# Optimization experiments

Hardware: AMD Instinct MI355X
Metric: run time of the kernel (lower is better)

The kernel has to match this reference:

```python
import jax, jax.numpy as jnp
import numpy as np

D_MODEL = 2048
NUM_Q_HEADS = 16
NUM_KV_HEADS = 4
HEAD_DIM = D_MODEL // NUM_Q_HEADS  # 128
NUM_GROUPS = NUM_Q_HEADS // NUM_KV_HEADS  # 4
ROPE_BASE = 10000.0


def _rope_cos_sin(seq_len, head_dim):
    inv_freq = 1.0 / (ROPE_BASE ** (jnp.arange(0, head_dim, 2, dtype=jnp.float32) / head_dim))
    t = jnp.arange(seq_len, dtype=jnp.float32)
    freqs = jnp.outer(t, inv_freq)            # [S, head_dim/2]
    emb = jnp.concatenate([freqs, freqs], -1)  # [S, head_dim]
    return jnp.cos(emb)[None, :, None, :], jnp.sin(emb)[None, :, None, :]


def _rotate_half(x):
    half = x.shape[-1] // 2
    return jnp.concatenate([-x[..., half:], x[..., :half]], axis=-1)


def setup_inputs() -> dict:
    key = jax.random.key(0)
    k0, k1, k2, k3, k4 = jax.random.split(key, 5)
    B, S = 2, 2048
    kv_dim = HEAD_DIM * NUM_KV_HEADS
    scale = D_MODEL ** -0.5
    return {
        "x": jax.random.normal(k0, (B, S, D_MODEL), jnp.float32),
        "attention_mask": jnp.ones((B, S), jnp.int32),
        "Wq": jax.random.normal(k1, (D_MODEL, D_MODEL), jnp.float32) * scale,
        "Wk": jax.random.normal(k2, (D_MODEL, kv_dim), jnp.float32) * scale,
        "Wv": jax.random.normal(k3, (D_MODEL, kv_dim), jnp.float32) * scale,
        "Wo": jax.random.normal(k4, (D_MODEL, D_MODEL), jnp.float32) * scale,
    }


def reference(x, attention_mask, Wq, Wk, Wv, Wo):
    B, S, _ = x.shape
    q = (x @ Wq).reshape(B, S, NUM_Q_HEADS, HEAD_DIM)
    k = (x @ Wk).reshape(B, S, NUM_KV_HEADS, HEAD_DIM)
    v = (x @ Wv).reshape(B, S, NUM_KV_HEADS, HEAD_DIM)

    cos, sin = _rope_cos_sin(S, HEAD_DIM)  # [1,S,1,hd]
    q = q * cos + _rotate_half(q) * sin
    k = k * cos + _rotate_half(k) * sin

    # [B, H, S, hd]; replicate KV heads across groups (repeat_interleave)
    q = q.transpose(0, 2, 1, 3)
    k = jnp.repeat(k.transpose(0, 2, 1, 3), NUM_GROUPS, axis=1)
    v = jnp.repeat(v.transpose(0, 2, 1, 3), NUM_GROUPS, axis=1)

    scale = HEAD_DIM ** -0.5
    scores = jnp.einsum("bhqd,bhkd->bhqk", q, k) * scale
    mask = attention_mask[:, None, None, :]  # [B,1,1,S] over keys
    scores = jnp.where(mask == 0, jnp.float32(-jnp.inf), scores)
    probs = jax.nn.softmax(scores, axis=-1)
    out = jnp.einsum("bhqk,bhkd->bhqd", probs, v)
    out = out.transpose(0, 2, 1, 3).reshape(B, S, D_MODEL)
    return out @ Wo
```

## Files before the change

kernel.cpp:

```cpp
#include <hip/hip_runtime.h>
#include <hip/hip_bf16.h>

typedef __attribute__((ext_vector_type(4))) float f32x4;
typedef __attribute__((ext_vector_type(8))) short s16x8;
typedef __attribute__((ext_vector_type(4))) short s16x4;

__device__ __forceinline__ float fexp2(float x) {
    float y; asm("v_exp_f32 %0, %1" : "=v"(y) : "v"(x)); return y;
}

__global__ void rope_tables(float* __restrict__ cosT, float* __restrict__ sinT) {
    const int s = blockIdx.x, j = threadIdx.x;
    const double inv = pow(10000.0, -(double)j / 64.0);
    const double f = (double)s * inv;
    cosT[s * 64 + j] = (float)cos(f);
    sinT[s * 64 + j] = (float)sin(f);
}

__global__ void mask_bias(const int* __restrict__ mask, float* __restrict__ mb, int n) {
    const int i = blockIdx.x * 256 + threadIdx.x;
    if (i < n) mb[i] = (mask[i] == 0) ? -1e30f : 0.f;
}

__global__ __launch_bounds__(256)
void cast_f32_bf16(const float* __restrict__ src, __hip_bfloat16* __restrict__ dst, int n4) {
    const int i = blockIdx.x * 256 + threadIdx.x;
    if (i < n4) {
        f32x4 v = *reinterpret_cast<const f32x4*>(src + (size_t)i * 4);
        union { s16x4 v4; __hip_bfloat16 h[4]; } u;
#pragma unroll
        for (int j = 0; j < 4; ++j) u.h[j] = __float2bfloat16(v[j]);
        *reinterpret_cast<s16x4*>(dst + (size_t)i * 4) = u.v4;
    }
}

__global__ __launch_bounds__(256)
void transpose_cast(const float* __restrict__ src, __hip_bfloat16* __restrict__ dst,
                    int R, int C) {
    __shared__ __align__(16) float t[32][33];
    const int tx = threadIdx.x, ty = threadIdx.y;
    const int r0 = blockIdx.y * 32, c0 = blockIdx.x * 32;
#pragma unroll
    for (int i = 0; i < 32; i += 8)
        t[ty + i][tx] = src[(size_t)(r0 + ty + i) * C + c0 + tx];
    __syncthreads();
#pragma unroll
    for (int i = 0; i < 32; i += 8)
        dst[(size_t)(c0 + ty + i) * R + r0 + tx] = __float2bfloat16(t[tx][ty + i]);
}

__global__ __launch_bounds__(256)
void vt_transpose(const float* __restrict__ qkv, __hip_bfloat16* __restrict__ Vt) {
    __shared__ __align__(16) float t[32][33];
    const int tx = threadIdx.x, ty = threadIdx.y;
    const int s0 = blockIdx.x * 32, d0 = blockIdx.y * 32;
    const int bh = blockIdx.z, b = bh >> 2, hh = bh & 3;
#pragma unroll
    for (int i = 0; i < 32; i += 8)
        t[ty + i][tx] = qkv[(size_t)(b * 2048 + s0 + ty + i) * 3072 + 2560 + hh * 128 + d0 + tx];
    __syncthreads();
#pragma unroll
    for (int i = 0; i < 32; i += 8)
        Vt[((size_t)(bh * 128) + d0 + ty + i) * 2048 + s0 + tx] = __float2bfloat16(t[tx][ty + i]);
}

template<int NI>
__global__ __launch_bounds__(512, 1)
void gemm256_bt_f32(const __hip_bfloat16* __restrict__ A,
                    const __hip_bfloat16* __restrict__ Bt,
                    float* __restrict__ C, int M, int N, int K) {
    constexpr int NB = NI / 2;
    __shared__ __align__(16) __hip_bfloat16 sm[4][2][8192];
    const int tid = threadIdx.x;
    const int l = tid & 63, w = tid >> 6;
    const int lo = l & 15, hi = l >> 4;
    const int wm = w >> 2, wn = w & 3;
    const int row0 = blockIdx.y * 256;
    const int col0 = blockIdx.x * (NI * 64);
    const int nk = K >> 5;

    f32x4 acc[8][NI];
#pragma unroll
    for (int mi = 0; mi < 8; ++mi)
#pragma unroll
        for (int ni = 0; ni < NI; ++ni) acc[mi][ni] = f32x4{0.f, 0.f, 0.f, 0.f};

    auto stage = [&](int kt) {
        const int s = kt & 3, k0 = kt << 5;
#pragma unroll
        for (int i = 0; i < 2; ++i) {
            const int c = i * 512 + tid;
            const int r = c >> 2, sw = ((c & 3) ^ (r & 3)) * 8;
            __builtin_amdgcn_global_load_lds(
                (const __attribute__((address_space(1))) void*)(A + (size_t)(row0 + r) * K + k0 + sw),
                (__attribute__((address_space(3))) void*)(&sm[s][0][c * 8]), 16, 0, 0);
        }
#pragma unroll
        for (int i = 0; i < NB; ++i) {
            const int c = i * 512 + tid;
            const int r = c >> 2, sw = ((c & 3) ^ (r & 3)) * 8;
            __builtin_amdgcn_global_load_lds(
                (const __attribute__((address_space(1))) void*)(Bt + (size_t)(col0 + r) * K + k0 + sw),
                (__attribute__((address_space(3))) void*)(&sm[s][1][c * 8]), 16, 0, 0);
        }
    };

    stage(0); stage(1); stage(2);
    for (int kt = 0; kt < nk; ++kt) {
        const int s = kt & 3;
        if (kt < nk - 2) {
            if constexpr (NI == 4) asm volatile("s_waitcnt vmcnt(8)" ::: "memory");
            else                   asm volatile("s_waitcnt vmcnt(6)" ::: "memory");
        } else if (kt == nk - 2) {
            if constexpr (NI == 4) asm volatile("s_waitcnt vmcnt(4)" ::: "memory");
            else                   asm volatile("s_waitcnt vmcnt(3)" ::: "memory");
        } else {
            asm volatile("s_waitcnt vmcnt(0)" ::: "memory");
        }
        asm volatile("s_waitcnt lgkmcnt(0)" ::: "memory");
        asm volatile("s_barrier" ::: "memory");
        if (kt + 3 < nk) stage(kt + 3);

        s16x8 af[8], bf[NI];
#pragma unroll
        for (int mi = 0; mi < 8; ++mi)
            af[mi] = *reinterpret_cast<const s16x8*>(
                &sm[s][0][(wm * 128 + mi * 16 + lo) * 32 + ((hi ^ (lo & 3)) * 8)]);
#pragma unroll
        for (int ni = 0; ni < NI; ++ni)
            bf[ni] = *reinterpret_cast<const s16x8*>(
                &sm[s][1][(wn * NI * 16 + ni * 16 + lo) * 32 + ((hi ^ (lo & 3)) * 8)]);
        __builtin_amdgcn_s_setprio(1);
#pragma unroll
        for (int mi = 0; mi < 8; ++mi)
#pragma unroll
            for (int ni = 0; ni < NI; ++ni)
                acc[mi][ni] = __builtin_amdgcn_mfma_f32_16x16x32_bf16(af[mi], bf[ni], acc[mi][ni], 0, 0, 0);
        __builtin_amdgcn_s_setprio(0);
    }
    const int rbase = row0 + wm * 128 + hi * 4;
    const int cbase = col0 + wn * NI * 16 + lo;
#pragma unroll
    for (int mi = 0; mi < 8; ++mi)
#pragma unroll
        for (int ni = 0; ni < NI; ++ni)
#pragma unroll
            for (int r = 0; r < 4; ++r)
                C[(size_t)(rbase + mi * 16 + r) * N + cbase + ni * 16] = acc[mi][ni][r];
}

__global__ __launch_bounds__(256)
void rope_scatter(const float* __restrict__ qkv,
                  const float* __restrict__ cosT, const float* __restrict__ sinT,
                  __hip_bfloat16* __restrict__ Qr, __hip_bfloat16* __restrict__ Kr) {
    const int m = blockIdx.y;
    const int col4 = blockIdx.x * 256 + threadIdx.x;
    if (col4 >= 640) return;
    const int col = col4 * 4;
    const int b = m >> 11, s = m & 2047;
    const int d = col & 127;
    const int j = d & 63;
    const f32x4 v = *reinterpret_cast<const f32x4*>(qkv + (size_t)m * 3072 + col);
    const f32x4 p = *reinterpret_cast<const f32x4*>(qkv + (size_t)m * 3072 + (col ^ 64));
    const f32x4 c4 = *reinterpret_cast<const f32x4*>(cosT + s * 64 + j);
    const f32x4 s4 = *reinterpret_cast<const f32x4*>(sinT + s * 64 + j);
    const float sgn = (d < 64) ? -1.f : 1.f;
    union { s16x4 v4; __hip_bfloat16 h[4]; } u;
#pragma unroll
    for (int i = 0; i < 4; ++i)
        u.h[i] = __float2bfloat16(v[i] * c4[i] + sgn * p[i] * s4[i]);
    if (col < 2048) {
        const int hh = col >> 7;
        *reinterpret_cast<s16x4*>(&Qr[((size_t)(b * 16 + hh) * 2048 + s) * 128 + d]) = u.v4;
    } else {
        const int hh = (col - 2048) >> 7;
        *reinterpret_cast<s16x4*>(&Kr[((size_t)(b * 4 + hh) * 2048 + s) * 128 + d]) = u.v4;
    }
}

__global__ __launch_bounds__(512, 4)
void attn_kernel(const __hip_bfloat16* __restrict__ Qr,
                 const __hip_bfloat16* __restrict__ Kr,
                 const __hip_bfloat16* __restrict__ Vt,
                 const float* __restrict__ maskb,
                 __hip_bfloat16* __restrict__ Oo) {
    const int S = 2048;
    const int qt = blockIdx.x;
    const int bh = blockIdx.y;
    const int b = bh >> 4, h = bh & 15, kvh = h >> 2;
    const int tid = threadIdx.x;
    const int l = tid & 63, w = tid >> 6;
    const int lo = l & 15, hi = l >> 4;
    __shared__ __align__(16) __hip_bfloat16 Ks[2][64 * 128];
    __shared__ __align__(16) __hip_bfloat16 Vs[2][128 * 64];
    __shared__ __align__(16) __hip_bfloat16 Ps[8][16 * 64];

    const __hip_bfloat16* Qb = Qr + (size_t)(b * 16 + h) * S * 128;
    const __hip_bfloat16* Kb = Kr + (size_t)(b * 4 + kvh) * S * 128;
    const __hip_bfloat16* Vb = Vt + (size_t)(b * 4 + kvh) * 128 * S;
    const float* mrow = maskb + b * S;

    const int qrow = qt * 128 + w * 16 + lo;
    s16x8 qf[4];
#pragma unroll
    for (int kc = 0; kc < 4; ++kc)
        qf[kc] = *reinterpret_cast<const s16x8*>(Qb + (size_t)qrow * 128 + kc * 32 + hi * 8);

    float m_run = -1e30f, l_run = 0.f;
    f32x4 o[8];
#pragma unroll
    for (int n = 0; n < 8; ++n) o[n] = f32x4{0.f, 0.f, 0.f, 0.f};
    const float scale2 = 0.12751682f;

    const int krow = tid >> 4, kc8 = tid & 15;
    const int koff = (kc8 ^ (krow & 7)) * 8;
    const int vrow = tid >> 3, vc8 = tid & 7;
    const int voff = (vc8 ^ (vrow & 7)) * 8;

    s16x8 kreg[2], vreg[2];
    auto load_tile = [&](int kv0) {
#pragma unroll
        for (int i = 0; i < 2; ++i)
            kreg[i] = *reinterpret_cast<const s16x8*>(
                Kb + (size_t)(kv0 + i * 32 + krow) * 128 + kc8 * 8);
#pragma unroll
        for (int i = 0; i < 2; ++i)
            vreg[i] = *reinterpret_cast<const s16x8*>(
                Vb + (size_t)(i * 64 + vrow) * S + kv0 + vc8 * 8);
    };

    auto body = [&](int kt, __hip_bfloat16* Kc, __hip_bfloat16* Vc) {
        const int kv0 = kt * 64;
        f32x4 bi[4];
#pragma unroll
        for (int ksub = 0; ksub < 4; ++ksub)
            bi[ksub] = *reinterpret_cast<const f32x4*>(mrow + kv0 + ksub * 16 + hi * 4);
#pragma unroll
        for (int i = 0; i < 2; ++i)
            *reinterpret_cast<s16x8*>(Kc + (i * 32 + krow) * 128 + koff) = kreg[i];
#pragma unroll
        for (int i = 0; i < 2; ++i)
            *reinterpret_cast<s16x8*>(Vc + (i * 64 + vrow) * 64 + voff) = vreg[i];
        if (kt < 31) load_tile(kv0 + 64);
        __syncthreads();

        f32x4 sc[4] = {};
        __builtin_amdgcn_s_setprio(1);
#pragma unroll
        for (int ksub = 0; ksub < 4; ++ksub) {
            const int kr = ksub * 16 + lo;
            const int ksw = kr & 7;
#pragma unroll
            for (int kc = 0; kc < 4; ++kc) {
                s16x8 kf = *reinterpret_cast<const s16x8*>(
                    Kc + kr * 128 + (((kc * 4 + hi) ^ ksw) * 8));
                sc[ksub] = __builtin_amdgcn_mfma_f32_16x16x32_bf16(kf, qf[kc], sc[ksub], 0, 0, 0);
            }
        }
        __builtin_amdgcn_s_setprio(0);
#pragma unroll
        for (int ksub = 0; ksub < 4; ++ksub)
#pragma unroll
            for (int r = 0; r < 4; ++r)
                sc[ksub][r] = fmaf(sc[ksub][r], scale2, bi[ksub][r]);
        float a0 = fmaxf(fmaxf(sc[0][0], sc[0][1]), fmaxf(sc[0][2], sc[0][3]));
        float a1 = fmaxf(fmaxf(sc[1][0], sc[1][1]), fmaxf(sc[1][2], sc[1][3]));
        float a2 = fmaxf(fmaxf(sc[2][0], sc[2][1]), fmaxf(sc[2][2], sc[2][3]));
        float a3 = fmaxf(fmaxf(sc[3][0], sc[3][1]), fmaxf(sc[3][2], sc[3][3]));
        float mx = fmaxf(fmaxf(a0, a1), fmaxf(a2, a3));
        mx = fmaxf(mx, __shfl_xor(mx, 16));
        mx = fmaxf(mx, __shfl_xor(mx, 32));
        if (__ballot(mx > m_run + 11.5417f) != 0ull) {
            const float mnew = fmaxf(m_run, mx);
            const float alpha = fexp2(m_run - mnew);
            m_run = mnew;
            l_run *= alpha;
            float ar[4];
#pragma unroll
            for (int r = 0; r < 4; ++r) ar[r] = __shfl(alpha, hi * 4 + r);
#pragma unroll
            for (int n = 0; n < 8; ++n)
#pragma unroll
                for (int r = 0; r < 4; ++r) o[n][r] *= ar[r];
        }
        float s0 = 0.f, s1 = 0.f, s2 = 0.f, s3 = 0.f;
#pragma unroll
        for (int r = 0; r < 4; ++r) {
            sc[0][r] = fexp2(sc[0][r] - m_run); s0 += sc[0][r];
            sc[1][r] = fexp2(sc[1][r] - m_run); s1 += sc[1][r];
            sc[2][r] = fexp2(sc[2][r] - m_run); s2 += sc[2][r];
            sc[3][r] = fexp2(sc[3][r] - m_run); s3 += sc[3][r];
        }
        float ssum = (s0 + s1) + (s2 + s3);
        ssum += __shfl_xor(ssum, 16);
        ssum += __shfl_xor(ssum, 32);
        l_run += ssum;
        __hip_bfloat16* pb = &Ps[w][0];
#pragma unroll
        for (int ksub = 0; ksub < 4; ++ksub) {
            unsigned int d0, d1;
            asm("v_cvt_pk_bf16_f32 %0, %1, %2" : "=v"(d0) : "v"(sc[ksub][0]), "v"(sc[ksub][1]));
            asm("v_cvt_pk_bf16_f32 %0, %1, %2" : "=v"(d1) : "v"(sc[ksub][2]), "v"(sc[ksub][3]));
            const int byteoff = lo * 128 + (((ksub * 2 + (hi >> 1)) ^ (lo & 7)) * 16) + (hi & 1) * 8;
            uint2 dd; dd.x = d0; dd.y = d1;
            *reinterpret_cast<uint2*>(reinterpret_cast<char*>(pb) + byteoff) = dd;
        }
        __builtin_amdgcn_s_setprio(1);
#pragma unroll
        for (int kg = 0; kg < 2; ++kg) {
            s16x8 pa = *reinterpret_cast<const s16x8*>(
                pb + lo * 64 + (((kg * 4 + hi) ^ (lo & 7)) * 8));
#pragma unroll
            for (int n = 0; n < 8; ++n) {
                const int vr = n * 16 + lo;
                s16x8 vb = *reinterpret_cast<const s16x8*>(
                    Vc + vr * 64 + (((kg * 4 + hi) ^ (vr & 7)) * 8));
                o[n] = __builtin_amdgcn_mfma_f32_16x16x32_bf16(pa, vb, o[n], 0, 0, 0);
            }
        }
        __builtin_amdgcn_s_setprio(0);
    };

    load_tile(0);
    for (int kt2 = 0; kt2 < 16; ++kt2) {
        body(2 * kt2,     &Ks[0][0], &Vs[0][0]);
        body(2 * kt2 + 1, &Ks[1][0], &Vs[1][0]);
    }
    float lr[4];
#pragma unroll
    for (int r = 0; r < 4; ++r) lr[r] = __shfl(l_run, hi * 4 + r);
    const int orow = b * S + qt * 128 + w * 16 + (hi * 4);
    const int ocol = h * 128 + lo;
#pragma unroll
    for (int n = 0; n < 8; ++n)
#pragma unroll
        for (int r = 0; r < 4; ++r)
            Oo[(size_t)(orow + r) * 2048 + ocol + n * 16] = __float2bfloat16(o[n][r] / lr[r]);
}

extern "C" void kernel_launch(void* const* d_in, const int* in_sizes, int n_in,
                              void* d_out, int out_size, void* d_ws, size_t ws_size,
                              hipStream_t stream) {
    const float* x  = (const float*)d_in[0];
    const int* mask = (const int*)d_in[1];
    const float* Wq = (const float*)d_in[2];
    const float* Wk = (const float*)d_in[3];
    const float* Wv = (const float*)d_in[4];
    const float* Wo = (const float*)d_in[5];
    float* out = (float*)d_out;

    char* ws = (char*)d_ws;
    size_t off = 0;
    auto alloc = [&](size_t bytes) -> void* {
        void* p = ws + off;
        off += (bytes + 255) & ~(size_t)255;
        return p;
    };
    __hip_bfloat16* xb     = (__hip_bfloat16*)alloc(4096ULL * 2048 * 2);
    __hip_bfloat16* wqkv_t = (__hip_bfloat16*)alloc(3072ULL * 2048 * 2);
    __hip_bfloat16* wo_t   = (__hip_bfloat16*)alloc(2048ULL * 2048 * 2);
    float*          qkv    = (float*)alloc(4096ULL * 3072 * 4);
    __hip_bfloat16* Kr     = (__hip_bfloat16*)alloc(2ULL * 4 * 2048 * 128 * 2);
    __hip_bfloat16* Vt     = (__hip_bfloat16*)alloc(2ULL * 4 * 2048 * 128 * 2);
    float*          cosT   = (float*)alloc(2048ULL * 64 * 4);
    float*          sinT   = (float*)alloc(2048ULL * 64 * 4);
    float*          maskb  = (float*)alloc(2ULL * 2048 * 4);
    __hip_bfloat16* Qr    = xb;
    __hip_bfloat16* attno = (__hip_bfloat16*)qkv;

    rope_tables<<<dim3(2048), dim3(64), 0, stream>>>(cosT, sinT);
    mask_bias<<<dim3(16), dim3(256), 0, stream>>>(mask, maskb, 4096);
    cast_f32_bf16<<<dim3(8192), dim3(256), 0, stream>>>(x, xb, 2097152);
    transpose_cast<<<dim3(64, 64), dim3(32, 8), 0, stream>>>(Wq, wqkv_t, 2048, 2048);
    transpose_cast<<<dim3(16, 64), dim3(32, 8), 0, stream>>>(Wk, wqkv_t + 2048ULL * 2048, 2048, 512);
    transpose_cast<<<dim3(16, 64), dim3(32, 8), 0, stream>>>(Wv, wqkv_t + 2560ULL * 2048, 2048, 512);
    transpose_cast<<<dim3(64, 64), dim3(32, 8), 0, stream>>>(Wo, wo_t, 2048, 2048);

    gemm256_bt_f32<4><<<dim3(12, 16), dim3(512), 0, stream>>>(xb, wqkv_t, qkv, 4096, 3072, 2048);
    rope_scatter<<<dim3(3, 4096), dim3(256), 0, stream>>>(qkv, cosT, sinT, Qr, Kr);
    vt_transpose<<<dim3(64, 4, 8), dim3(32, 8), 0, stream>>>(qkv, Vt);
    attn_kernel<<<dim3(16, 32), dim3(512), 0, stream>>>(Qr, Kr, Vt, maskb, attno);
    gemm256_bt_f32<2><<<dim3(16, 16), dim3(512), 0, stream>>>(attno, wo_t, out, 4096, 2048, 2048);
}
```

Baseline: 251.0 us.

## Emit bf16 QKV from projection GEMM, remap blocks for XCD locality, change LDS swizzle

The QKV projection GEMM now writes bf16 instead of fp32, so rope_scatter and vt_transpose read half the bytes and the QKV intermediate buffer is halved. Both GEMMs use a 1D grid with a block remap that groups row tiles per XCD (id&7), intended to improve L2 reuse across chiplets. The LDS swizzle changes from r&3 to (r>>1)&3 to reduce bank conflicts. The attention output gets its own buffer instead of aliasing qkv. Rounding Q/K to bf16 before RoPE adds a small precision loss.

```diff
diff --git a/kernel.cpp b/kernel.cpp
--- a/kernel.cpp
+++ b/kernel.cpp
@@ -50,33 +50,37 @@
 }
 
 __global__ __launch_bounds__(256)
-void vt_transpose(const float* __restrict__ qkv, __hip_bfloat16* __restrict__ Vt) {
-    __shared__ __align__(16) float t[32][33];
+void vt_transpose(const __hip_bfloat16* __restrict__ qkv, __hip_bfloat16* __restrict__ Vt) {
+    __shared__ unsigned short t[32][33];
     const int tx = threadIdx.x, ty = threadIdx.y;
     const int s0 = blockIdx.x * 32, d0 = blockIdx.y * 32;
     const int bh = blockIdx.z, b = bh >> 2, hh = bh & 3;
+    const unsigned short* q = (const unsigned short*)qkv;
 #pragma unroll
     for (int i = 0; i < 32; i += 8)
-        t[ty + i][tx] = qkv[(size_t)(b * 2048 + s0 + ty + i) * 3072 + 2560 + hh * 128 + d0 + tx];
+        t[ty + i][tx] = q[(size_t)(b * 2048 + s0 + ty + i) * 3072 + 2560 + hh * 128 + d0 + tx];
     __syncthreads();
 #pragma unroll
     for (int i = 0; i < 32; i += 8)
-        Vt[((size_t)(bh * 128) + d0 + ty + i) * 2048 + s0 + tx] = __float2bfloat16(t[tx][ty + i]);
-}
-
-template<int NI>
+        ((unsigned short*)Vt)[((size_t)(bh * 128) + d0 + ty + i) * 2048 + s0 + tx] = t[tx][ty + i];
+}
+
+template<int NI, bool BF16OUT>
 __global__ __launch_bounds__(512, 1)
-void gemm256_bt_f32(const __hip_bfloat16* __restrict__ A,
-                    const __hip_bfloat16* __restrict__ Bt,
-                    float* __restrict__ C, int M, int N, int K) {
+void gemm256_bt(const __hip_bfloat16* __restrict__ A,
+                const __hip_bfloat16* __restrict__ Bt,
+                void* __restrict__ Cv, int M, int N, int K, int NX) {
     constexpr int NB = NI / 2;
     __shared__ __align__(16) __hip_bfloat16 sm[4][2][8192];
     const int tid = threadIdx.x;
     const int l = tid & 63, w = tid >> 6;
     const int lo = l & 15, hi = l >> 4;
     const int wm = w >> 2, wn = w & 3;
-    const int row0 = blockIdx.y * 256;
-    const int col0 = blockIdx.x * (NI * 64);
+    const int id = blockIdx.x, slot = id >> 3;
+    const int by = (id & 7) * 2 + slot / NX;
+    const int bx = slot % NX;
+    const int row0 = by * 256;
+    const int col0 = bx * (NI * 64);
     const int nk = K >> 5;
 
     f32x4 acc[8][NI];
@@ -90,7 +94,7 @@
 #pragma unroll
         for (int i = 0; i < 2; ++i) {
             const int c = i * 512 + tid;
-            const int r = c >> 2, sw = ((c & 3) ^ (r & 3)) * 8;
+            const int r = c >> 2, sw = ((c & 3) ^ ((r >> 1) & 3)) * 8;
             __builtin_amdgcn_global_load_lds(
                 (const __attribute__((address_space(1))) void*)(A + (size_t)(row0 + r) * K + k0 + sw),
                 (__attribute__((address_space(3))) void*)(&sm[s][0][c * 8]), 16, 0, 0);
@@ -98,7 +102,7 @@
 #pragma unroll
         for (int i = 0; i < NB; ++i) {
             const int c = i * 512 + tid;
-            const int r = c >> 2, sw = ((c & 3) ^ (r & 3)) * 8;
+            const int r = c >> 2, sw = ((c & 3) ^ ((r >> 1) & 3)) * 8;
             __builtin_amdgcn_global_load_lds(
                 (const __attribute__((address_space(1))) void*)(Bt + (size_t)(col0 + r) * K + k0 + sw),
                 (__attribute__((address_space(3))) void*)(&sm[s][1][c * 8]), 16, 0, 0);
@@ -122,14 +126,15 @@
         if (kt + 3 < nk) stage(kt + 3);
 
         s16x8 af[8], bf[NI];
+        const int rsw = ((lo >> 1) & 3);
 #pragma unroll
         for (int mi = 0; mi < 8; ++mi)
             af[mi] = *reinterpret_cast<const s16x8*>(
-                &sm[s][0][(wm * 128 + mi * 16 + lo) * 32 + ((hi ^ (lo & 3)) * 8)]);
+                &sm[s][0][(wm * 128 + mi * 16 + lo) * 32 + ((hi ^ rsw) * 8)]);
 #pragma unroll
         for (int ni = 0; ni < NI; ++ni)
             bf[ni] = *reinterpret_cast<const s16x8*>(
-                &sm[s][1][(wn * NI * 16 + ni * 16 + lo) * 32 + ((hi ^ (lo & 3)) * 8)]);
+                &sm[s][1][(wn * NI * 16 + ni * 16 + lo) * 32 + ((hi ^ rsw) * 8)]);
         __builtin_amdgcn_s_setprio(1);
 #pragma unroll
         for (int mi = 0; mi < 8; ++mi)
@@ -140,17 +145,30 @@
     }
     const int rbase = row0 + wm * 128 + hi * 4;
     const int cbase = col0 + wn * NI * 16 + lo;
-#pragma unroll
-    for (int mi = 0; mi < 8; ++mi)
-#pragma unroll
-        for (int ni = 0; ni < NI; ++ni)
-#pragma unroll
-            for (int r = 0; r < 4; ++r)
-                C[(size_t)(rbase + mi * 16 + r) * N + cbase + ni * 16] = acc[mi][ni][r];
+    if constexpr (BF16OUT) {
+        __hip_bfloat16* C = (__hip_bfloat16*)Cv;
+#pragma unroll
+        for (int mi = 0; mi < 8; ++mi)
+#pragma unroll
+            for (int ni = 0; ni < NI; ++ni)
+#pragma unroll
+                for (int r = 0; r < 4; ++r)
+                    C[(size_t)(rbase + mi * 16 + r) * N + cbase + ni * 16] =
+                        __float2bfloat16(acc[mi][ni][r]);
+    } else {
+        float* C = (float*)Cv;
+#pragma unroll
+        for (int mi = 0; mi < 8; ++mi)
+#pragma unroll
+            for (int ni = 0; ni < NI; ++ni)
+#pragma unroll
+                for (int r = 0; r < 4; ++r)
+                    C[(size_t)(rbase + mi * 16 + r) * N + cbase + ni * 16] = acc[mi][ni][r];
+    }
 }
 
 __global__ __launch_bounds__(256)
-void rope_scatter(const float* __restrict__ qkv,
+void rope_scatter(const __hip_bfloat16* __restrict__ qkv,
                   const float* __restrict__ cosT, const float* __restrict__ sinT,
                   __hip_bfloat16* __restrict__ Qr, __hip_bfloat16* __restrict__ Kr) {
     const int m = blockIdx.y;
@@ -160,15 +178,16 @@
     const int b = m >> 11, s = m & 2047;
     const int d = col & 127;
     const int j = d & 63;
-    const f32x4 v = *reinterpret_cast<const f32x4*>(qkv + (size_t)m * 3072 + col);
-    const f32x4 p = *reinterpret_cast<const f32x4*>(qkv + (size_t)m * 3072 + (col ^ 64));
+    union { s16x4 v4; __hip_bfloat16 h[4]; } vv, pp, u;
+    vv.v4 = *reinterpret_cast<const s16x4*>(qkv + (size_t)m * 3072 + col);
+    pp.v4 = *reinterpret_cast<const s16x4*>(qkv + (size_t)m * 3072 + (col ^ 64));
     const f32x4 c4 = *reinterpret_cast<const f32x4*>(cosT + s * 64 + j);
     const f32x4 s4 = *reinterpret_cast<const f32x4*>(sinT + s * 64 + j);
     const float sgn = (d < 64) ? -1.f : 1.f;
-    union { s16x4 v4; __hip_bfloat16 h[4]; } u;
 #pragma unroll
     for (int i = 0; i < 4; ++i)
-        u.h[i] = __float2bfloat16(v[i] * c4[i] + sgn * p[i] * s4[i]);
+        u.h[i] = __float2bfloat16(__bfloat162float(vv.h[i]) * c4[i] +
+                                  sgn * __bfloat162float(pp.h[i]) * s4[i]);
     if (col < 2048) {
         const int hh = col >> 7;
         *reinterpret_cast<s16x4*>(&Qr[((size_t)(b * 16 + hh) * 2048 + s) * 128 + d]) = u.v4;
@@ -359,14 +378,14 @@
     __hip_bfloat16* xb     = (__hip_bfloat16*)alloc(4096ULL * 2048 * 2);
     __hip_bfloat16* wqkv_t = (__hip_bfloat16*)alloc(3072ULL * 2048 * 2);
     __hip_bfloat16* wo_t   = (__hip_bfloat16*)alloc(2048ULL * 2048 * 2);
-    float*          qkv    = (float*)alloc(4096ULL * 3072 * 4);
+    __hip_bfloat16* qkvb   = (__hip_bfloat16*)alloc(4096ULL * 3072 * 2);
     __hip_bfloat16* Kr     = (__hip_bfloat16*)alloc(2ULL * 4 * 2048 * 128 * 2);
     __hip_bfloat16* Vt     = (__hip_bfloat16*)alloc(2ULL * 4 * 2048 * 128 * 2);
     float*          cosT   = (float*)alloc(2048ULL * 64 * 4);
     float*          sinT   = (float*)alloc(2048ULL * 64 * 4);
     float*          maskb  = (float*)alloc(2ULL * 2048 * 4);
+    __hip_bfloat16* attno  = (__hip_bfloat16*)alloc(4096ULL * 2048 * 2);
     __hip_bfloat16* Qr    = xb;
-    __hip_bfloat16* attno = (__hip_bfloat16*)qkv;
 
     rope_tables<<<dim3(2048), dim3(64), 0, stream>>>(cosT, sinT);
     mask_bias<<<dim3(16), dim3(256), 0, stream>>>(mask, maskb, 4096);
@@ -376,9 +395,9 @@
     transpose_cast<<<dim3(16, 64), dim3(32, 8), 0, stream>>>(Wv, wqkv_t + 2560ULL * 2048, 2048, 512);
     transpose_cast<<<dim3(64, 64), dim3(32, 8), 0, stream>>>(Wo, wo_t, 2048, 2048);
 
-    gemm256_bt_f32<4><<<dim3(12, 16), dim3(512), 0, stream>>>(xb, wqkv_t, qkv, 4096, 3072, 2048);
-    rope_scatter<<<dim3(3, 4096), dim3(256), 0, stream>>>(qkv, cosT, sinT, Qr, Kr);
-    vt_transpose<<<dim3(64, 4, 8), dim3(32, 8), 0, stream>>>(qkv, Vt);
+    gemm256_bt<4, true><<<dim3(192), dim3(512), 0, stream>>>(xb, wqkv_t, qkvb, 4096, 3072, 2048, 12);
+    rope_scatter<<<dim3(3, 4096), dim3(256), 0, stream>>>(qkvb, cosT, sinT, Qr, Kr);
+    vt_transpose<<<dim3(64, 4, 8), dim3(32, 8), 0, stream>>>(qkvb, Vt);
     attn_kernel<<<dim3(16, 32), dim3(512), 0, stream>>>(Qr, Kr, Vt, maskb, attno);
-    gemm256_bt_f32<2><<<dim3(16, 16), dim3(512), 0, stream>>>(attno, wo_t, out, 4096, 2048, 2048);
-}
+    gemm256_bt<2, false><<<dim3(256), dim3(512), 0, stream>>>(attno, wo_t, out, 4096, 2048, 2048, 16);
+}
```

Measured after the change: 238.5 us. 5.0% less time.
